# Kernel optimization log

Measured on AMD Instinct MI355X. Metric: run time of the kernel, lower is better.

Reference implementation:

```python
import jax, jax.numpy as jnp
import numpy as np

PI = np.pi
N_PTS = 2_000_000
IMG_H, IMG_W = 1024, 2048


def cloud2idx(xyz):
    # spherical projection of 3D points to panorama coords in [-1, 1]
    phi = jnp.arctan2(xyz[:, 1], xyz[:, 0]) + PI          # horizontal angle in [0, 2pi]
    theta = jnp.arctan2(jnp.linalg.norm(xyz[:, :2], axis=-1), xyz[:, 2])  # vertical in [0, pi]
    cx = 2.0 * (1.0 - phi / (2.0 * PI)) - 1.0
    cy = 2.0 * (theta / PI) - 1.0
    return jnp.stack([cx, cy], axis=-1)                   # (N, 2)


def sample_from_img(img, coords):
    # bilinear grid_sample, align_corners=False, border padding
    H, W = img.shape[0], img.shape[1]
    x = jnp.clip((coords[:, 0] + 1.0) * 0.5 * W - 0.5, 0.0, W - 1.0)
    y = jnp.clip((coords[:, 1] + 1.0) * 0.5 * H - 0.5, 0.0, H - 1.0)
    x0 = jnp.floor(x); y0 = jnp.floor(y)
    wx = (x - x0)[:, None]; wy = (y - y0)[:, None]
    x0i = x0.astype(jnp.int32); y0i = y0.astype(jnp.int32)
    x1i = jnp.minimum(x0i + 1, W - 1); y1i = jnp.minimum(y0i + 1, H - 1)
    v00 = img[y0i, x0i]; v01 = img[y0i, x1i]
    v10 = img[y1i, x0i]; v11 = img[y1i, x1i]
    return (v00 * (1 - wx) * (1 - wy) + v01 * wx * (1 - wy)
            + v10 * (1 - wx) * wy + v11 * wx * wy)        # (N, C)


def rot_matrix(yaw, pitch, roll):
    cy, sy = jnp.cos(yaw)[0], jnp.sin(yaw)[0]
    cp, sp = jnp.cos(pitch)[0], jnp.sin(pitch)[0]
    cr, sr = jnp.cos(roll)[0], jnp.sin(roll)[0]
    one = jnp.float32(1.0); zero = jnp.float32(0.0)
    RX = jnp.stack([jnp.stack([one, zero, zero]),
                    jnp.stack([zero, cr, -sr]),
                    jnp.stack([zero, sr, cr])])
    RY = jnp.stack([jnp.stack([cp, zero, sp]),
                    jnp.stack([zero, one, zero]),
                    jnp.stack([-sp, zero, cp])])
    RZ = jnp.stack([jnp.stack([cy, -sy, zero]),
                    jnp.stack([sy, cy, zero]),
                    jnp.stack([zero, zero, one])])
    return RZ @ RY @ RX


def setup_inputs() -> dict:
    key = jax.random.key(0)
    ks = jax.random.split(key, 9)
    return {
        "translation": jax.random.normal(ks[0], (3, 1), jnp.float32),
        "yaw": jax.random.normal(ks[1], (1,), jnp.float32),
        "pitch": jax.random.normal(ks[2], (1,), jnp.float32),
        "roll": jax.random.normal(ks[3], (1,), jnp.float32),
        "xyz": jax.random.normal(ks[4], (N_PTS, 3), jnp.float32),
        "rgb": jax.random.uniform(ks[5], (N_PTS, 3), jnp.float32),
        "img": jax.random.uniform(ks[6], (IMG_H, IMG_W, 3), jnp.float32),
        "img_weight": jax.random.uniform(ks[7], (IMG_H, IMG_W, 1), jnp.float32),
        "pcd_weight": jax.random.uniform(ks[8], (N_PTS,), jnp.float32),
    }


def reference(translation, yaw, pitch, roll, xyz, rgb, img, img_weight, pcd_weight):
    R = rot_matrix(yaw, pitch, roll)                      # (3, 3)
    new_xyz = (R @ (xyz.T - translation)).T               # (N, 3)
    coord_arr = cloud2idx(new_xyz)                        # (N, 2)
    sample_rgb = sample_from_img(img, coord_arr)          # (N, 3)
    raw_loss = jnp.linalg.norm(sample_rgb - rgb, axis=-1) # (N,)
    # img_weight is sampled under no_grad in the original
    w_img = jax.lax.stop_gradient(sample_from_img(img_weight, coord_arr))[:, 0]
    raw_loss = 0.5 * (w_img + pcd_weight) * raw_loss
    mask = jnp.sum(sample_rgb == 0, axis=1) != 3          # (N,) bool
    return (raw_loss * mask).sum() / mask.sum().astype(jnp.float32)
```

## Files before the change

kernel.cpp:

```cpp
#include <hip/hip_runtime.h>
#include <math.h>

#define PI_F 3.14159265358979323846f

constexpr int IMG_H = 1024;
constexpr int IMG_W = 2048;
constexpr int BLOCK = 256;
constexpr int GRID  = 2048;

constexpr size_t PARTIALS_BYTES = 64 * 1024;
constexpr size_t PAIR_BYTES = (size_t)IMG_H * IMG_W * 8;

typedef float f32x4 __attribute__((ext_vector_type(4)));
typedef float f32x2 __attribute__((ext_vector_type(2), aligned(4)));
typedef unsigned int u32x4 __attribute__((ext_vector_type(4), aligned(8)));

__device__ __forceinline__ unsigned pack_unorm8(float r, float g, float b, float w) {
    const unsigned ur = (unsigned)(r * 255.0f + 0.5f);
    const unsigned ug = (unsigned)(g * 255.0f + 0.5f);
    const unsigned ub = (unsigned)(b * 255.0f + 0.5f);
    const unsigned uw = (unsigned)(w * 255.0f + 0.5f);
    return ur | (ug << 8) | (ub << 16) | (uw << 24);
}
__device__ __forceinline__ float ub0(unsigned u) { return (float)(unsigned char)(u); }
__device__ __forceinline__ float ub1(unsigned u) { return (float)(unsigned char)(u >> 8); }
__device__ __forceinline__ float ub2(unsigned u) { return (float)(unsigned char)(u >> 16); }
__device__ __forceinline__ float ub3(unsigned u) { return (float)(u >> 24); }

__global__ __launch_bounds__(BLOCK) void pair_pack(
    const f32x4* __restrict__ img4,
    const f32x4* __restrict__ imgw4,
    unsigned* __restrict__ P)
{
    const int g = blockIdx.x * BLOCK + threadIdx.x;
    const int QW = IMG_W / 4;
    if (g >= IMG_H * QW) return;
    const int y  = g / QW;
    const int q  = g - y * QW;
    const int yb = min(y + 1, IMG_H - 1);

    const int qa = y * QW + q;
    const int qb = yb * QW + q;

    const f32x4 a0 = img4[3 * qa + 0];
    const f32x4 a1 = img4[3 * qa + 1];
    const f32x4 a2 = img4[3 * qa + 2];
    const f32x4 wa = imgw4[qa];
    const f32x4 b0 = img4[3 * qb + 0];
    const f32x4 b1 = img4[3 * qb + 1];
    const f32x4 b2 = img4[3 * qb + 2];
    const f32x4 wb = imgw4[qb];

    const unsigned t0 = pack_unorm8(a0.x, a0.y, a0.z, wa.x);
    const unsigned t1 = pack_unorm8(a0.w, a1.x, a1.y, wa.y);
    const unsigned t2 = pack_unorm8(a1.z, a1.w, a2.x, wa.z);
    const unsigned t3 = pack_unorm8(a2.y, a2.z, a2.w, wa.w);
    const unsigned u0 = pack_unorm8(b0.x, b0.y, b0.z, wb.x);
    const unsigned u1 = pack_unorm8(b0.w, b1.x, b1.y, wb.y);
    const unsigned u2 = pack_unorm8(b1.z, b1.w, b2.x, wb.z);
    const unsigned u3 = pack_unorm8(b2.y, b2.z, b2.w, wb.w);

    u32x4* out = (u32x4*)(P + (size_t)2 * (y * IMG_W + 4 * q));
    u32x4 w0; w0.x = t0; w0.y = u0; w0.z = t1; w0.w = u1;
    u32x4 w1; w1.x = t2; w1.y = u2; w1.z = t3; w1.w = u3;
    out[0] = w0;
    out[1] = w1;
}

__global__ __launch_bounds__(BLOCK) void sampling_loss_pair(
    const float* __restrict__ translation,
    const float* __restrict__ yaw,
    const float* __restrict__ pitch,
    const float* __restrict__ roll,
    const float* __restrict__ xyz,
    const float* __restrict__ rgb,
    const unsigned* __restrict__ P,
    const float* __restrict__ pcdw,
    double* __restrict__ partials,
    int N)
{
    const float cyw = cosf(yaw[0]),   syw = sinf(yaw[0]);
    const float cpw = cosf(pitch[0]), spw = sinf(pitch[0]);
    const float crw = cosf(roll[0]),  srw = sinf(roll[0]);

    const float R00 = cyw * cpw;
    const float R01 = -syw * crw + cyw * spw * srw;
    const float R02 =  syw * srw + cyw * spw * crw;
    const float R10 =  syw * cpw;
    const float R11 =  cyw * crw + syw * spw * srw;
    const float R12 = -cyw * srw + syw * spw * crw;
    const float R20 = -spw;
    const float R21 =  cpw * srw;
    const float R22 =  cpw * crw;

    const float tx = translation[0], ty = translation[1], tz = translation[2];
    const float inv255 = 1.0f / 255.0f;

    double acc_loss = 0.0;
    double acc_mask = 0.0;

    for (int i = blockIdx.x * BLOCK + threadIdx.x; i < N; i += GRID * BLOCK) {
        const f32x2 xy  = __builtin_nontemporal_load((const f32x2*)&xyz[3 * i]);
        const float zz  = __builtin_nontemporal_load(&xyz[3 * i + 2]);
        const f32x2 cc  = __builtin_nontemporal_load((const f32x2*)&rgb[3 * i]);
        const float cb2 = __builtin_nontemporal_load(&rgb[3 * i + 2]);
        const float pw  = __builtin_nontemporal_load(&pcdw[i]);

        const float px = xy.x - tx;
        const float py = xy.y - ty;
        const float pz = zz   - tz;

        const float nx = R00 * px + R01 * py + R02 * pz;
        const float ny = R10 * px + R11 * py + R12 * pz;
        const float nz = R20 * px + R21 * py + R22 * pz;

        const float phi   = atan2f(ny, nx) + PI_F;
        const float theta = atan2f(sqrtf(nx * nx + ny * ny), nz);
        const float cx  = 2.0f * (1.0f - phi / (2.0f * PI_F)) - 1.0f;
        const float cyv = 2.0f * (theta / PI_F) - 1.0f;

        float fx = (cx + 1.0f) * 0.5f * (float)IMG_W - 0.5f;
        float fy = (cyv + 1.0f) * 0.5f * (float)IMG_H - 0.5f;
        fx = fminf(fmaxf(fx, 0.0f), (float)(IMG_W - 1));
        fy = fminf(fmaxf(fy, 0.0f), (float)(IMG_H - 1));

        const float x0f = floorf(fx), y0f = floorf(fy);
        const float wx = fx - x0f,    wy = fy - y0f;
        const int x0 = (int)x0f, y0 = (int)y0f;

        const int bx = min(x0, IMG_W - 2);
        const bool shx = (x0 != bx);
        const u32x4 v = *(const u32x4*)(P + (size_t)2 * (y0 * IMG_W + bx));

        const unsigned u00 = shx ? v.z : v.x;
        const unsigned u01 = v.z;
        const unsigned u10 = shx ? v.w : v.y;
        const unsigned u11 = v.w;

        const float w00 = (1.0f - wx) * (1.0f - wy);
        const float w01 = wx * (1.0f - wy);
        const float w10 = (1.0f - wx) * wy;
        const float w11 = wx * wy;

        const float r8 = w00 * ub0(u00) + w01 * ub0(u01) + w10 * ub0(u10) + w11 * ub0(u11);
        const float g8 = w00 * ub1(u00) + w01 * ub1(u01) + w10 * ub1(u10) + w11 * ub1(u11);
        const float b8 = w00 * ub2(u00) + w01 * ub2(u01) + w10 * ub2(u10) + w11 * ub2(u11);
        const float w8 = w00 * ub3(u00) + w01 * ub3(u01) + w10 * ub3(u10) + w11 * ub3(u11);

        const float s0 = r8 * inv255;
        const float s1 = g8 * inv255;
        const float s2 = b8 * inv255;
        const float wimg = w8 * inv255;

        const float dr = s0 - cc.x;
        const float dg = s1 - cc.y;
        const float db = s2 - cb2;
        const float raw = sqrtf(dr * dr + dg * dg + db * db);

        const bool mask = !((r8 == 0.0f) && (g8 == 0.0f) && (b8 == 0.0f));

        if (mask) {
            acc_loss += (double)(0.5f * (wimg + pw) * raw);
            acc_mask += 1.0;
        }
    }

    for (int off = 32; off > 0; off >>= 1) {
        acc_loss += __shfl_down(acc_loss, off);
        acc_mask += __shfl_down(acc_mask, off);
    }
    __shared__ double sL[BLOCK / 64];
    __shared__ double sM[BLOCK / 64];
    const int lane = threadIdx.x & 63;
    const int wave = threadIdx.x >> 6;
    if (lane == 0) { sL[wave] = acc_loss; sM[wave] = acc_mask; }
    __syncthreads();
    if (threadIdx.x == 0) {
        double L = 0.0, M = 0.0;
        for (int w = 0; w < BLOCK / 64; ++w) { L += sL[w]; M += sM[w]; }
        partials[2 * blockIdx.x + 0] = L;
        partials[2 * blockIdx.x + 1] = M;
    }
}

__global__ __launch_bounds__(BLOCK) void sampling_loss_partial(
    const float* __restrict__ translation,
    const float* __restrict__ yaw,
    const float* __restrict__ pitch,
    const float* __restrict__ roll,
    const float* __restrict__ xyz,
    const float* __restrict__ rgb,
    const float* __restrict__ img,
    const float* __restrict__ imgw,
    const float* __restrict__ pcdw,
    double* __restrict__ partials,
    int N)
{
    const float cyw = cosf(yaw[0]),   syw = sinf(yaw[0]);
    const float cpw = cosf(pitch[0]), spw = sinf(pitch[0]);
    const float crw = cosf(roll[0]),  srw = sinf(roll[0]);
    const float R00 = cyw * cpw;
    const float R01 = -syw * crw + cyw * spw * srw;
    const float R02 =  syw * srw + cyw * spw * crw;
    const float R10 =  syw * cpw;
    const float R11 =  cyw * crw + syw * spw * srw;
    const float R12 = -cyw * srw + syw * spw * crw;
    const float R20 = -spw;
    const float R21 =  cpw * srw;
    const float R22 =  cpw * crw;
    const float tx = translation[0], ty = translation[1], tz = translation[2];

    double acc_loss = 0.0, acc_mask = 0.0;
    for (int i = blockIdx.x * BLOCK + threadIdx.x; i < N; i += GRID * BLOCK) {
        const float px = xyz[3 * i + 0] - tx;
        const float py = xyz[3 * i + 1] - ty;
        const float pz = xyz[3 * i + 2] - tz;
        const float nx = R00 * px + R01 * py + R02 * pz;
        const float ny = R10 * px + R11 * py + R12 * pz;
        const float nz = R20 * px + R21 * py + R22 * pz;
        const float phi   = atan2f(ny, nx) + PI_F;
        const float theta = atan2f(sqrtf(nx * nx + ny * ny), nz);
        const float cx = 2.0f * (1.0f - phi / (2.0f * PI_F)) - 1.0f;
        const float cyv = 2.0f * (theta / PI_F) - 1.0f;
        float fx = (cx + 1.0f) * 0.5f * (float)IMG_W - 0.5f;
        float fy = (cyv + 1.0f) * 0.5f * (float)IMG_H - 0.5f;
        fx = fminf(fmaxf(fx, 0.0f), (float)(IMG_W - 1));
        fy = fminf(fmaxf(fy, 0.0f), (float)(IMG_H - 1));
        const float x0f = floorf(fx), y0f = floorf(fy);
        const float wx = fx - x0f,    wy = fy - y0f;
        const int x0 = (int)x0f, y0 = (int)y0f;
        const int x1 = min(x0 + 1, IMG_W - 1);
        const int y1 = min(y0 + 1, IMG_H - 1);
        const float w00 = (1.0f - wx) * (1.0f - wy);
        const float w01 = wx * (1.0f - wy);
        const float w10 = (1.0f - wx) * wy;
        const float w11 = wx * wy;
        const float* p00 = img + (size_t)(y0 * IMG_W + x0) * 3;
        const float* p01 = img + (size_t)(y0 * IMG_W + x1) * 3;
        const float* p10 = img + (size_t)(y1 * IMG_W + x0) * 3;
        const float* p11 = img + (size_t)(y1 * IMG_W + x1) * 3;
        const float s0 = w00 * p00[0] + w01 * p01[0] + w10 * p10[0] + w11 * p11[0];
        const float s1 = w00 * p00[1] + w01 * p01[1] + w10 * p10[1] + w11 * p11[1];
        const float s2 = w00 * p00[2] + w01 * p01[2] + w10 * p10[2] + w11 * p11[2];
        const float wimg = w00 * imgw[y0 * IMG_W + x0] + w01 * imgw[y0 * IMG_W + x1]
                         + w10 * imgw[y1 * IMG_W + x0] + w11 * imgw[y1 * IMG_W + x1];
        const float dr = s0 - rgb[3 * i + 0];
        const float dg = s1 - rgb[3 * i + 1];
        const float db = s2 - rgb[3 * i + 2];
        const float raw = sqrtf(dr * dr + dg * dg + db * db);
        const bool mask = !((s0 == 0.0f) && (s1 == 0.0f) && (s2 == 0.0f));
        const float li = 0.5f * (wimg + pcdw[i]) * raw;
        if (mask) { acc_loss += (double)li; acc_mask += 1.0; }
    }
    for (int off = 32; off > 0; off >>= 1) {
        acc_loss += __shfl_down(acc_loss, off);
        acc_mask += __shfl_down(acc_mask, off);
    }
    __shared__ double sL[BLOCK / 64];
    __shared__ double sM[BLOCK / 64];
    const int lane = threadIdx.x & 63;
    const int wave = threadIdx.x >> 6;
    if (lane == 0) { sL[wave] = acc_loss; sM[wave] = acc_mask; }
    __syncthreads();
    if (threadIdx.x == 0) {
        double L = 0.0, M = 0.0;
        for (int w = 0; w < BLOCK / 64; ++w) { L += sL[w]; M += sM[w]; }
        partials[2 * blockIdx.x + 0] = L;
        partials[2 * blockIdx.x + 1] = M;
    }
}

__global__ __launch_bounds__(BLOCK) void sampling_loss_finalize(
    const double* __restrict__ partials, float* __restrict__ out, int nBlocks)
{
    double L = 0.0, M = 0.0;
    for (int i = threadIdx.x; i < nBlocks; i += BLOCK) {
        L += partials[2 * i + 0];
        M += partials[2 * i + 1];
    }
    for (int off = 32; off > 0; off >>= 1) {
        L += __shfl_down(L, off);
        M += __shfl_down(M, off);
    }
    __shared__ double sL[BLOCK / 64];
    __shared__ double sM[BLOCK / 64];
    const int lane = threadIdx.x & 63;
    const int wave = threadIdx.x >> 6;
    if (lane == 0) { sL[wave] = L; sM[wave] = M; }
    __syncthreads();
    if (threadIdx.x == 0) {
        double tl = 0.0, tm = 0.0;
        for (int w = 0; w < BLOCK / 64; ++w) { tl += sL[w]; tm += sM[w]; }
        out[0] = (float)(tl / tm);
    }
}

extern "C" void kernel_launch(void* const* d_in, const int* in_sizes, int n_in,
                              void* d_out, int out_size, void* d_ws, size_t ws_size,
                              hipStream_t stream) {
    const float* translation = (const float*)d_in[0];
    const float* yaw         = (const float*)d_in[1];
    const float* pitch       = (const float*)d_in[2];
    const float* roll        = (const float*)d_in[3];
    const float* xyz         = (const float*)d_in[4];
    const float* rgb         = (const float*)d_in[5];
    const float* img         = (const float*)d_in[6];
    const float* imgw        = (const float*)d_in[7];
    const float* pcdw        = (const float*)d_in[8];

    const int N = in_sizes[8];

    double* partials = (double*)d_ws;
    float* out = (float*)d_out;

    if (ws_size >= PARTIALS_BYTES + PAIR_BYTES) {
        unsigned* P = (unsigned*)((char*)d_ws + PARTIALS_BYTES);
        const int packThreads = IMG_H * (IMG_W / 4);
        pair_pack<<<(packThreads + BLOCK - 1) / BLOCK, BLOCK, 0, stream>>>(
            (const f32x4*)img, (const f32x4*)imgw, P);

        sampling_loss_pair<<<GRID, BLOCK, 0, stream>>>(
            translation, yaw, pitch, roll, xyz, rgb, P, pcdw, partials, N);
    } else {
        sampling_loss_partial<<<GRID, BLOCK, 0, stream>>>(
            translation, yaw, pitch, roll, xyz, rgb, img, imgw, pcdw, partials, N);
    }
    sampling_loss_finalize<<<1, BLOCK, 0, stream>>>(partials, out, GRID);
}
```

Measured before the change: 48.52 us.

## Use polynomial atan2 in turns and split texture packing into two passes

Replaces the libm atan2f calls with a minimax polynomial atan2 that returns turns, folding the spherical-to-pixel mapping into fewer operations. The texture preparation is split into a unorm pack kernel that reads each pixel once, followed by a row-pairing kernel that interleaves adjacent rows from the compact 32-bit texture. The two-pass split avoids reading the float image twice but adds a kernel launch and an intermediate buffer. The polynomial approximation could shift sample positions slightly.

```diff
diff --git a/kernel.cpp b/kernel.cpp
--- a/kernel.cpp
+++ b/kernel.cpp
@@ -1,7 +1,5 @@
 #include <hip/hip_runtime.h>
 #include <math.h>
-
-#define PI_F 3.14159265358979323846f
 
 constexpr int IMG_H = 1024;
 constexpr int IMG_W = 2048;
@@ -9,11 +7,14 @@
 constexpr int GRID  = 2048;
 
 constexpr size_t PARTIALS_BYTES = 64 * 1024;
-constexpr size_t PAIR_BYTES = (size_t)IMG_H * IMG_W * 8;
+constexpr size_t PAIR_BYTES   = (size_t)IMG_H * IMG_W * 8;
+constexpr size_t TEXU32_BYTES = (size_t)IMG_H * IMG_W * 4;
 
 typedef float f32x4 __attribute__((ext_vector_type(4)));
-typedef float f32x2 __attribute__((ext_vector_type(2), aligned(4)));
+typedef float f32x2a __attribute__((ext_vector_type(2), aligned(4)));
 typedef unsigned int u32x4 __attribute__((ext_vector_type(4), aligned(8)));
+
+#define PI_F 3.14159265358979323846f
 
 __device__ __forceinline__ unsigned pack_unorm8(float r, float g, float b, float w) {
     const unsigned ur = (unsigned)(r * 255.0f + 0.5f);
@@ -27,7 +28,68 @@
 __device__ __forceinline__ float ub2(unsigned u) { return (float)(unsigned char)(u >> 16); }
 __device__ __forceinline__ float ub3(unsigned u) { return (float)(u >> 24); }
 
-__global__ __launch_bounds__(BLOCK) void pair_pack(
+__device__ __forceinline__ float atan_turns_poly(float a) {
+    const float s = a * a;
+    float p = -0.001865487f;
+    p = p * s + 0.008380035f;
+    p = p * s - 0.018530866f;
+    p = p * s + 0.030803399f;
+    p = p * s - 0.05293865f;
+    p = p * s + 0.15915132f;
+    return p * a;
+}
+
+__device__ __forceinline__ float atan2_turns(float y, float x) {
+    const float ax = fabsf(x), ay = fabsf(y);
+    const float mx = fmaxf(ax, ay), mn = fminf(ax, ay);
+    const float a = mn * __builtin_amdgcn_rcpf(mx);
+    float r = atan_turns_poly(a);
+    r = (ay > ax) ? (0.25f - r) : r;
+    r = (x < 0.0f) ? (0.5f - r) : r;
+    return (y < 0.0f) ? -r : r;
+}
+
+__global__ __launch_bounds__(BLOCK) void pack_unorm(
+    const f32x4* __restrict__ img4,
+    const f32x4* __restrict__ imgw4,
+    uint4* __restrict__ T4)
+{
+    const int g = blockIdx.x * BLOCK + threadIdx.x;
+    if (g >= IMG_H * IMG_W / 4) return;
+    const f32x4 a = img4[3 * g + 0];
+    const f32x4 b = img4[3 * g + 1];
+    const f32x4 c = img4[3 * g + 2];
+    const f32x4 w = imgw4[g];
+    uint4 t;
+    t.x = pack_unorm8(a.x, a.y, a.z, w.x);
+    t.y = pack_unorm8(a.w, b.x, b.y, w.y);
+    t.z = pack_unorm8(b.z, b.w, c.x, w.z);
+    t.w = pack_unorm8(c.y, c.z, c.w, w.w);
+    T4[g] = t;
+}
+
+__global__ __launch_bounds__(BLOCK) void pair_rows(
+    const uint4* __restrict__ T4,
+    unsigned* __restrict__ P)
+{
+    const int g = blockIdx.x * BLOCK + threadIdx.x;
+    const int QW = IMG_W / 4;
+    if (g >= IMG_H * QW) return;
+    const int y  = g / QW;
+    const int q  = g - y * QW;
+    const int y1 = min(y + 1, IMG_H - 1);
+
+    const uint4 a = T4[y * QW + q];
+    const uint4 b = T4[y1 * QW + q];
+
+    uint4 lo; lo.x = a.x; lo.y = b.x; lo.z = a.y; lo.w = b.y;
+    uint4 hi; hi.x = a.z; hi.y = b.z; hi.z = a.w; hi.w = b.w;
+    uint4* out = (uint4*)(P + (size_t)2 * (y * IMG_W + 4 * q));
+    out[0] = lo;
+    out[1] = hi;
+}
+
+__global__ __launch_bounds__(BLOCK) void pair_pack_direct(
     const f32x4* __restrict__ img4,
     const f32x4* __restrict__ imgw4,
     unsigned* __restrict__ P)
@@ -38,7 +100,6 @@
     const int y  = g / QW;
     const int q  = g - y * QW;
     const int yb = min(y + 1, IMG_H - 1);
-
     const int qa = y * QW + q;
     const int qb = yb * QW + q;
 
@@ -60,14 +121,14 @@
     const unsigned u2 = pack_unorm8(b1.z, b1.w, b2.x, wb.z);
     const unsigned u3 = pack_unorm8(b2.y, b2.z, b2.w, wb.w);
 
-    u32x4* out = (u32x4*)(P + (size_t)2 * (y * IMG_W + 4 * q));
-    u32x4 w0; w0.x = t0; w0.y = u0; w0.z = t1; w0.w = u1;
-    u32x4 w1; w1.x = t2; w1.y = u2; w1.z = t3; w1.w = u3;
-    out[0] = w0;
-    out[1] = w1;
-}
-
-__global__ __launch_bounds__(BLOCK) void sampling_loss_pair(
+    uint4 lo; lo.x = t0; lo.y = u0; lo.z = t1; lo.w = u1;
+    uint4 hi; hi.x = t2; hi.y = u2; hi.z = t3; hi.w = u3;
+    uint4* out = (uint4*)(P + (size_t)2 * (y * IMG_W + 4 * q));
+    out[0] = lo;
+    out[1] = hi;
+}
+
+__global__ __launch_bounds__(BLOCK) void sampling_loss_pair2(
     const float* __restrict__ translation,
     const float* __restrict__ yaw,
     const float* __restrict__ pitch,
@@ -100,11 +161,11 @@
     double acc_mask = 0.0;
 
     for (int i = blockIdx.x * BLOCK + threadIdx.x; i < N; i += GRID * BLOCK) {
-        const f32x2 xy  = __builtin_nontemporal_load((const f32x2*)&xyz[3 * i]);
-        const float zz  = __builtin_nontemporal_load(&xyz[3 * i + 2]);
-        const f32x2 cc  = __builtin_nontemporal_load((const f32x2*)&rgb[3 * i]);
-        const float cb2 = __builtin_nontemporal_load(&rgb[3 * i + 2]);
-        const float pw  = __builtin_nontemporal_load(&pcdw[i]);
+        const f32x2a xy  = __builtin_nontemporal_load((const f32x2a*)&xyz[3 * i]);
+        const float zz   = __builtin_nontemporal_load(&xyz[3 * i + 2]);
+        const f32x2a cc  = __builtin_nontemporal_load((const f32x2a*)&rgb[3 * i]);
+        const float cb2  = __builtin_nontemporal_load(&rgb[3 * i + 2]);
+        const float pw   = __builtin_nontemporal_load(&pcdw[i]);
 
         const float px = xy.x - tx;
         const float py = xy.y - ty;
@@ -114,13 +175,12 @@
         const float ny = R10 * px + R11 * py + R12 * pz;
         const float nz = R20 * px + R21 * py + R22 * pz;
 
-        const float phi   = atan2f(ny, nx) + PI_F;
-        const float theta = atan2f(sqrtf(nx * nx + ny * ny), nz);
-        const float cx  = 2.0f * (1.0f - phi / (2.0f * PI_F)) - 1.0f;
-        const float cyv = 2.0f * (theta / PI_F) - 1.0f;
-
-        float fx = (cx + 1.0f) * 0.5f * (float)IMG_W - 0.5f;
-        float fy = (cyv + 1.0f) * 0.5f * (float)IMG_H - 0.5f;
+        const float t_phi = atan2_turns(ny, nx);
+        const float rxy   = sqrtf(nx * nx + ny * ny);
+        const float t_th  = atan2_turns(rxy, nz);
+
+        float fx = (0.5f - t_phi) * (float)IMG_W - 0.5f;
+        float fy = t_th * (2.0f * (float)IMG_H) - 0.5f;
         fx = fminf(fmaxf(fx, 0.0f), (float)(IMG_W - 1));
         fy = fminf(fmaxf(fy, 0.0f), (float)(IMG_H - 1));
 
@@ -147,20 +207,15 @@
         const float b8 = w00 * ub2(u00) + w01 * ub2(u01) + w10 * ub2(u10) + w11 * ub2(u11);
         const float w8 = w00 * ub3(u00) + w01 * ub3(u01) + w10 * ub3(u10) + w11 * ub3(u11);
 
-        const float s0 = r8 * inv255;
-        const float s1 = g8 * inv255;
-        const float s2 = b8 * inv255;
-        const float wimg = w8 * inv255;
-
-        const float dr = s0 - cc.x;
-        const float dg = s1 - cc.y;
-        const float db = s2 - cb2;
+        const float dr = r8 * inv255 - cc.x;
+        const float dg = g8 * inv255 - cc.y;
+        const float db = b8 * inv255 - cb2;
         const float raw = sqrtf(dr * dr + dg * dg + db * db);
 
         const bool mask = !((r8 == 0.0f) && (g8 == 0.0f) && (b8 == 0.0f));
 
         if (mask) {
-            acc_loss += (double)(0.5f * (wimg + pw) * raw);
+            acc_loss += (double)(0.5f * (w8 * inv255 + pw) * raw);
             acc_mask += 1.0;
         }
     }
@@ -211,7 +266,7 @@
     const float tx = translation[0], ty = translation[1], tz = translation[2];
 
     double acc_loss = 0.0, acc_mask = 0.0;
-    for (int i = blockIdx.x * BLOCK + threadIdx.x; i < N; i += GRID * BLOCK) {
+    for (int i = blockIdx.x * BLOCK + threadIdx.x; i < N; i += gridDim.x * BLOCK) {
         const float px = xyz[3 * i + 0] - tx;
         const float py = xyz[3 * i + 1] - ty;
         const float pz = xyz[3 * i + 2] - tz;
@@ -313,17 +368,29 @@
     double* partials = (double*)d_ws;
     float* out = (float*)d_out;
 
-    if (ws_size >= PARTIALS_BYTES + PAIR_BYTES) {
+    const int QW = IMG_W / 4;
+    const int quadThreads = IMG_H * QW;
+    const int texThreads  = IMG_H * IMG_W / 4;
+
+    if (ws_size >= PARTIALS_BYTES + PAIR_BYTES + TEXU32_BYTES) {
         unsigned* P = (unsigned*)((char*)d_ws + PARTIALS_BYTES);
-        const int packThreads = IMG_H * (IMG_W / 4);
-        pair_pack<<<(packThreads + BLOCK - 1) / BLOCK, BLOCK, 0, stream>>>(
+        uint4* T4   = (uint4*)((char*)d_ws + PARTIALS_BYTES + PAIR_BYTES);
+        pack_unorm<<<(texThreads + BLOCK - 1) / BLOCK, BLOCK, 0, stream>>>(
+            (const f32x4*)img, (const f32x4*)imgw, T4);
+        pair_rows<<<(quadThreads + BLOCK - 1) / BLOCK, BLOCK, 0, stream>>>(T4, P);
+        sampling_loss_pair2<<<GRID, BLOCK, 0, stream>>>(
+            translation, yaw, pitch, roll, xyz, rgb, P, pcdw, partials, N);
+        sampling_loss_finalize<<<1, BLOCK, 0, stream>>>(partials, out, GRID);
+    } else if (ws_size >= PARTIALS_BYTES + PAIR_BYTES) {
+        unsigned* P = (unsigned*)((char*)d_ws + PARTIALS_BYTES);
+        pair_pack_direct<<<(quadThreads + BLOCK - 1) / BLOCK, BLOCK, 0, stream>>>(
             (const f32x4*)img, (const f32x4*)imgw, P);
-
-        sampling_loss_pair<<<GRID, BLOCK, 0, stream>>>(
+        sampling_loss_pair2<<<GRID, BLOCK, 0, stream>>>(
             translation, yaw, pitch, roll, xyz, rgb, P, pcdw, partials, N);
+        sampling_loss_finalize<<<1, BLOCK, 0, stream>>>(partials, out, GRID);
     } else {
         sampling_loss_partial<<<GRID, BLOCK, 0, stream>>>(
             translation, yaw, pitch, roll, xyz, rgb, img, imgw, pcdw, partials, N);
-    }
-    sampling_loss_finalize<<<1, BLOCK, 0, stream>>>(partials, out, GRID);
-}
+        sampling_loss_finalize<<<1, BLOCK, 0, stream>>>(partials, out, GRID);
+    }
+}
```

Result: slower. 50.44 us (+3.9%).
